# Optimization experiments

Hardware: AMD Instinct MI355X
Metric: run time of the kernel (lower is better)

Reference implementation:

```python
import jax, jax.numpy as jnp
import numpy as np

B, S, H, D, E = 1, 2048, 16, 64, 1024
STRIDE, LCMP = 16, 32          # compression stride / block
LSEL, TOPN = 64, 16            # selection block size / top-k blocks
WIN = 512                      # sliding window
NEG = jnp.float32(-1e9)


def setup_inputs() -> dict:
    key = jax.random.key(0)
    ks = jax.random.split(key, 5)
    q = jax.random.normal(ks[0], (B, S, H, D), jnp.float32)
    k = jax.random.normal(ks[1], (B, S, H, D), jnp.float32)
    v = jax.random.normal(ks[2], (B, S, H, D), jnp.float32)
    x = jax.random.normal(ks[3], (B, S, E), jnp.float32)
    Wg = jax.random.normal(ks[4], (E, 3), jnp.float32) * 0.02
    bg = jnp.zeros((3,), jnp.float32)
    cu_seqlens = jnp.array([0, S], jnp.int32)
    max_seqlen = S
    return {"q": q, "k": k, "v": v, "x": x, "Wg": Wg, "bg": bg,
            "cu_seqlens": cu_seqlens, "max_seqlen": max_seqlen}


def _nsa_forward(q, k, v, x, Wg, bg):
    scale = 1.0 / np.sqrt(D)
    t = jnp.arange(S)
    num_cmp = (S - LCMP) // STRIDE + 1   # 127
    num_sel = S // LSEL                  # 32

    # ---- branch 1: compressed-KV attention (mean-pooled blocks) ----
    starts = jnp.arange(num_cmp) * STRIDE
    widx = starts[:, None] + jnp.arange(LCMP)          # (num_cmp, LCMP)
    Kc = k[:, widx].mean(axis=2)                        # (B, num_cmp, H, D)
    Vc = v[:, widx].mean(axis=2)
    logits_c = jnp.einsum('bshd,bchd->bhsc', q, Kc) * scale
    # query t may attend only to fully-past compressed blocks
    mask_c = (starts + LCMP)[None, :] <= (t[:, None] + 1)   # (S, num_cmp)
    p_c = jax.nn.softmax(jnp.where(mask_c[None, None], logits_c, NEG), axis=-1)
    valid_c = mask_c.any(axis=-1).astype(q.dtype)           # (S,) zero-out empty rows
    p_c = p_c * valid_c[None, None, :, None]
    o_cmp = jnp.einsum('bhsc,bchd->bshd', p_c, Vc)

    # ---- branch 2: top-k selected-block attention ----
    # map compressed-block scores -> selection-block importance (overlap sum)
    sel_s = jnp.arange(num_sel) * LSEL
    overlap = ((starts[:, None] < sel_s[None, :] + LSEL) &
               (starts[:, None] + LCMP > sel_s[None, :])).astype(q.dtype)  # (num_cmp, num_sel)
    p_sel = jnp.einsum('bhsc,cn->bhsn', p_c, overlap)        # (B,H,S,num_sel)
    _, top_idx = jax.lax.top_k(p_sel, TOPN)                  # (B,H,S,TOPN)
    sel_blk = jax.nn.one_hot(top_idx, num_sel).sum(axis=-2) > 0   # (B,H,S,num_sel)
    own_blk = jax.nn.one_hot(t // LSEL, num_sel) > 0              # always include own block
    sel_blk = sel_blk | own_blk[None, None]
    sel_tok = jnp.repeat(sel_blk, LSEL, axis=-1)             # (B,H,S,S) token-level mask

    causal = t[:, None] >= t[None, :]                        # (S,S)
    logits = jnp.einsum('bshd,bthd->bhst', q, k) * scale     # (B,H,S,S), shared by 2 branches
    a_sel = jax.nn.softmax(jnp.where(sel_tok & causal[None, None], logits, NEG), axis=-1)
    o_sel = jnp.einsum('bhst,bthd->bshd', a_sel, v)

    # ---- branch 3: sliding-window attention ----
    win_mask = causal & (t[:, None] - t[None, :] < WIN)
    a_win = jax.nn.softmax(jnp.where(win_mask[None, None], logits, NEG), axis=-1)
    o_win = jnp.einsum('bhst,bthd->bshd', a_win, v)

    # ---- learned gating over the 3 branches ----
    g = jax.nn.sigmoid(x @ Wg + bg)                          # (B,S,3)
    out = (g[..., 0][..., None, None] * o_cmp +
           g[..., 1][..., None, None] * o_sel +
           g[..., 2][..., None, None] * o_win)
    return out                                               # (B,S,H,D)


def reference(q, k, v, x, Wg, bg, cu_seqlens, max_seqlen):
    return _nsa_forward(q, k, v, x, Wg, bg)
```

## Files before the change

### kernel.cpp

```cpp
#include <hip/hip_runtime.h>
#include <hip/hip_bf16.h>
#include <math.h>

#define H_NUM 16
#define D_DIM 64
#define S_LEN 2048
#define E_DIM 1024
#define NC    127
#define TOPN  16
#define SCALE 0.125f
#define FIXM  16.0f
#define LOG2E 1.4426950408889634f
#define C_SC  (SCALE * LOG2E)
#define C_BI  (-FIXM * LOG2E)

typedef short s16x8 __attribute__((ext_vector_type(8)));
typedef short s16x4 __attribute__((ext_vector_type(4)));
typedef float f32x4 __attribute__((ext_vector_type(4)));
typedef unsigned short ushort_t;

__device__ __forceinline__ float fast_exp2(float x) {
    return __builtin_amdgcn_exp2f(x);
}
__device__ __forceinline__ unsigned short f2b(float f) {
    __hip_bfloat16 h = __float2bfloat16(f);
    return *reinterpret_cast<unsigned short*>(&h);
}
__device__ __forceinline__ float b2f(unsigned short u) {
    __hip_bfloat16 h = *reinterpret_cast<__hip_bfloat16*>(&u);
    return __bfloat162float(h);
}
__device__ __forceinline__ s16x8 pack8(float4 a, float4 b) {
    s16x8 r;
    r[0] = (short)f2b(a.x); r[1] = (short)f2b(a.y);
    r[2] = (short)f2b(a.z); r[3] = (short)f2b(a.w);
    r[4] = (short)f2b(b.x); r[5] = (short)f2b(b.y);
    r[6] = (short)f2b(b.z); r[7] = (short)f2b(b.w);
    return r;
}
__device__ __forceinline__ f32x4 mfma16(s16x8 a, s16x8 b, f32x4 c) {
    return __builtin_amdgcn_mfma_f32_16x16x32_bf16(a, b, c, 0, 0, 0);
}
__device__ __forceinline__ void wave_lds_fence() {
    asm volatile("s_waitcnt lgkmcnt(0)" ::: "memory");
    __builtin_amdgcn_sched_barrier(0);
}
__device__ __forceinline__ int swP(int r, int c) { return r * 128 + (c ^ ((r & 7) << 2)); }
__device__ __forceinline__ int swU(int r, int c) { return r * 64  + (c ^ ((r & 7) << 3)); }

__device__ __forceinline__ float wave_sum(float v) {
#pragma unroll
    for (int off = 32; off; off >>= 1) v += __shfl_xor(v, off, 64);
    return v;
}

__global__ __launch_bounds__(256) void nsa_prep(
    const float* __restrict__ k, const float* __restrict__ v,
    const float* __restrict__ x, const float* __restrict__ Wg, const float* __restrict__ bg,
    ushort_t* __restrict__ Kb, ushort_t* __restrict__ VtB,
    ushort_t* __restrict__ KcHi, ushort_t* __restrict__ KcLo, ushort_t* __restrict__ VcT,
    float* __restrict__ g)
{
    const int b   = blockIdx.x;
    const int tid = threadIdx.x;

    if (b < 512) {
        int idx0 = (b * 256 + tid) * 16;
#pragma unroll
        for (int j = 0; j < 16; j += 4) {
            int id = idx0 + j;
            int d = id & 63, s = (id >> 6) & 2047, h = id >> 17;
            float4 f = *(const float4*)(k + ((size_t)s * H_NUM + h) * D_DIM + d);
            s16x4 u;
            u[0] = (short)f2b(f.x); u[1] = (short)f2b(f.y);
            u[2] = (short)f2b(f.z); u[3] = (short)f2b(f.w);
            *(s16x4*)(Kb + id) = u;
        }
    } else if (b < 768) {
        __shared__ ushort_t T[64][136];
        int bb = b - 512;
        int h = bb >> 4, s0 = (bb & 15) << 7;
#pragma unroll
        for (int rep = 0; rep < 8; ++rep) {
            int idx = rep * 256 + tid;
            int i = idx >> 4, d4 = (idx & 15) << 2;
            float4 f = *(const float4*)(v + ((size_t)(s0 + i) * H_NUM + h) * D_DIM + d4);
            T[d4 + 0][i] = f2b(f.x); T[d4 + 1][i] = f2b(f.y);
            T[d4 + 2][i] = f2b(f.z); T[d4 + 3][i] = f2b(f.w);
        }
        __syncthreads();
        int d = tid >> 2, i0 = (tid & 3) << 5;
        ushort_t* dst = VtB + ((size_t)h * 64 + d) * 2048 + s0 + i0;
#pragma unroll
        for (int jj = 0; jj < 32; jj += 8)
            *(s16x8*)(dst + jj) = *(const s16x8*)&T[d][i0 + jj];
    } else if (b < 1280) {
        int unit = (b - 768) * 4 + (tid >> 6);
        int h = unit >> 7, c = unit & 127;
        int lane = tid & 63;
        float mk = 0.f, mv = 0.f;
        if (c < NC) {
            int s0 = c * 16;
#pragma unroll 4
            for (int i = 0; i < 32; ++i) {
                mk += k[((size_t)(s0 + i) * H_NUM + h) * D_DIM + lane];
                mv += v[((size_t)(s0 + i) * H_NUM + h) * D_DIM + lane];
            }
            mk *= (1.f / 32.f); mv *= (1.f / 32.f);
        }
        unsigned short khi = f2b(mk);
        KcHi[((size_t)h * 128 + c) * 64 + lane] = khi;
        KcLo[((size_t)h * 128 + c) * 64 + lane] = f2b(mk - b2f(khi));
        VcT[((size_t)h * 64 + lane) * 128 + c] = f2b(mv);
    } else {
        int s = (b - 1280) * 4 + (tid >> 6);
        int lane = tid & 63;
        float a0 = 0.f, a1 = 0.f, a2 = 0.f;
        for (int i = lane; i < E_DIM; i += 64) {
            float xv = x[(size_t)s * E_DIM + i];
            a0 = fmaf(xv, Wg[i * 3 + 0], a0);
            a1 = fmaf(xv, Wg[i * 3 + 1], a1);
            a2 = fmaf(xv, Wg[i * 3 + 2], a2);
        }
        a0 = wave_sum(a0); a1 = wave_sum(a1); a2 = wave_sum(a2);
        if (lane == 0) {
            g[s * 3 + 0] = 1.f / (1.f + expf(-(a0 + bg[0])));
            g[s * 3 + 1] = 1.f / (1.f + expf(-(a1 + bg[1])));
            g[s * 3 + 2] = 1.f / (1.f + expf(-(a2 + bg[2])));
        }
    }
}

__global__ __launch_bounds__(512, 4) void nsa_main(
    const float* __restrict__ q,
    const ushort_t* __restrict__ Kb, const ushort_t* __restrict__ VtB,
    const ushort_t* __restrict__ KcHi, const ushort_t* __restrict__ KcLo,
    const ushort_t* __restrict__ VcT,
    const float* __restrict__ gat, float* __restrict__ out)
{
    __shared__ __align__(16) float    P1[4 * 2048];
    __shared__ __align__(16) float    psl[4 * 512];
    __shared__ __align__(16) ushort_t BP[4 * 2048];
    __shared__ float    mrg[4 * 32];
    __shared__ unsigned selm_l[64];

    const int bid  = blockIdx.x;
    const int h    = bid & 15;
    const int grp  = bid >> 4;
    const int tile = (grp < 16) ? (31 - grp) : (grp - 16);
    const int t0   = tile << 6;
    const int tid  = threadIdx.x;
    const int w    = tid >> 6;
    const int pair = w & 3;
    const bool isA = w < 4;
    const int lane = tid & 63;
    const int lr   = lane & 15;
    const int g    = lane >> 4;
    const int rb   = t0 + 16 * pair;

    float*    P1w  = P1 + pair * 2048;
    float*    pslw = psl + pair * 512;
    ushort_t* APb  = (ushort_t*)pslw;
    ushort_t* BPw  = BP + pair * 2048;
    float*    mrgw = mrg + pair * 32;

    int trow[4];
#pragma unroll
    for (int r = 0; r < 4; ++r) trow[r] = rb + 4 * g + r;

    s16x8 qa[2], ql[2];
    {
        const float* qrow = q + ((size_t)(rb + lr) * H_NUM + h) * D_DIM;
#pragma unroll
        for (int kk = 0; kk < 2; ++kk) {
            float4 a = *(const float4*)(qrow + kk * 32 + g * 8);
            float4 b = *(const float4*)(qrow + kk * 32 + g * 8 + 4);
            s16x8 hi = pack8(a, b);
            float4 ar, br;
            ar.x = a.x - b2f((unsigned short)hi[0]); ar.y = a.y - b2f((unsigned short)hi[1]);
            ar.z = a.z - b2f((unsigned short)hi[2]); ar.w = a.w - b2f((unsigned short)hi[3]);
            br.x = b.x - b2f((unsigned short)hi[4]); br.y = b.y - b2f((unsigned short)hi[5]);
            br.z = b.z - b2f((unsigned short)hi[6]); br.w = b.w - b2f((unsigned short)hi[7]);
            qa[kk] = hi;
            ql[kk] = pack8(ar, br);
        }
    }

    int nv[4];
#pragma unroll
    for (int r = 0; r < 4; ++r) nv[r] = (trow[r] >= 31) ? (((trow[r] - 31) >> 4) + 1) : 0;

    float l1[4] = {0.f, 0.f, 0.f, 0.f};
    f32x4 oc[4];
#pragma unroll
    for (int dt = 0; dt < 4; ++dt) { f32x4 z = {0.f, 0.f, 0.f, 0.f}; oc[dt] = z; }

    const int winlo = (tile >= 8) ? (tile - 8) : 0;
    float l3[4] = {0.f, 0.f, 0.f, 0.f};
    f32x4 o3[4];
#pragma unroll
    for (int dt = 0; dt < 4; ++dt) { f32x4 z = {0.f, 0.f, 0.f, 0.f}; o3[dt] = z; }

    if (isA) {
        f32x4 sc8[8];
#pragma unroll
        for (int ct = 0; ct < 8; ++ct) {
            f32x4 acc = {0.f, 0.f, 0.f, 0.f};
#pragma unroll
            for (int kk = 0; kk < 2; ++kk) {
                const size_t off = ((size_t)h * 128 + 16 * ct + lr) * 64 + kk * 32 + g * 8;
                s16x8 khi = *(const s16x8*)(KcHi + off);
                s16x8 klo = *(const s16x8*)(KcLo + off);
                acc = mfma16(qa[kk], khi, acc);
                acc = mfma16(ql[kk], khi, acc);
                acc = mfma16(qa[kk], klo, acc);
            }
            sc8[ct] = acc;
        }

#pragma unroll
        for (int ct = 0; ct < 8; ++ct)
#pragma unroll
            for (int r = 0; r < 4; ++r) {
                int c = 16 * ct + lr;
                float p = (c < nv[r]) ? fast_exp2(fmaf(sc8[ct][r], C_SC, C_BI)) : 0.f;
                l1[r] += p;
                P1w[swP(4 * g + r, 16 * ct + lr)] = p;
            }
        wave_lds_fence();

#pragma unroll
        for (int rep = 0; rep < 8; ++rep) {
            int item = rep * 64 + lane;
            int n = item >> 4, row = item & 15;
            int lo = 4 * n - 1; if (lo < 0) lo = 0;
            int hi = 4 * n + 3; if (hi > NC - 1) hi = NC - 1;
            float s = 0.f;
            for (int c = lo; c <= hi; ++c) s += P1w[swP(row, c)];
            pslw[n * 16 + row] = s;
        }
        wave_lds_fence();

        unsigned mymask = 0u;
        {
            float pv[32];
#pragma unroll
            for (int n = 0; n < 32; ++n) pv[n] = (lane < 16) ? pslw[n * 16 + lane] : 0.f;
            for (int it = 0; it < TOPN; ++it) {
                float best = -1.f; int bi = 0;
#pragma unroll
                for (int n = 0; n < 32; ++n) {
                    float val = ((mymask >> n) & 1u) ? -2.f : pv[n];
                    if (val > best) { best = val; bi = n; }
                }
                mymask |= 1u << bi;
            }
        }
        if (lane < 16) selm_l[pair * 16 + lane] = mymask | (1u << tile);

#pragma unroll
        for (int kk = 0; kk < 4; ++kk) {
            float4 a0 = *(const float4*)&P1w[swP(lr, kk * 32 + g * 8)];
            float4 a1 = *(const float4*)&P1w[swP(lr, kk * 32 + g * 8 + 4)];
            s16x8 pa = pack8(a0, a1);
#pragma unroll
            for (int dt = 0; dt < 4; ++dt)
                oc[dt] = mfma16(pa, *(const s16x8*)(VcT + ((size_t)h * 64 + 16 * dt + lr) * 128 + kk * 32 + g * 8), oc[dt]);
        }
#pragma unroll
        for (int off = 8; off >= 1; off >>= 1)
#pragma unroll
            for (int r = 0; r < 4; ++r) l1[r] += __shfl_xor(l1[r], off, 64);
    } else {
        for (int n = winlo; n <= tile; ++n) {
            const int base = n << 6;
            f32x4 s4[4];
#pragma unroll
            for (int ct = 0; ct < 4; ++ct) {
                f32x4 acc = {0.f, 0.f, 0.f, 0.f};
#pragma unroll
                for (int kk = 0; kk < 2; ++kk)
                    acc = mfma16(qa[kk],
                        *(const s16x8*)(Kb + ((size_t)h * 2048 + base + 16 * ct + lr) * 64 + kk * 32 + g * 8), acc);
                s4[ct] = acc;
            }
#pragma unroll
            for (int ct = 0; ct < 4; ++ct)
#pragma unroll
                for (int r = 0; r < 4; ++r) {
                    int j = base + 16 * ct + lr;
                    bool ok = (j >= trow[r] - 511) && (j <= trow[r]);
                    float p = ok ? fast_exp2(fmaf(s4[ct][r], C_SC, C_BI)) : 0.f;
                    l3[r] += p;
                    BPw[swU(4 * g + r, 16 * ct + lr)] = f2b(p);
                }
            wave_lds_fence();
#pragma unroll
            for (int kk = 0; kk < 2; ++kk) {
                s16x8 pa = *(const s16x8*)&BPw[swU(lr, kk * 32 + g * 8)];
#pragma unroll
                for (int dt = 0; dt < 4; ++dt)
                    o3[dt] = mfma16(pa,
                        *(const s16x8*)(VtB + ((size_t)h * 64 + 16 * dt + lr) * 2048 + base + kk * 32 + g * 8), o3[dt]);
            }
        }
#pragma unroll
        for (int off = 8; off >= 1; off >>= 1)
#pragma unroll
            for (int r = 0; r < 4; ++r) l3[r] += __shfl_xor(l3[r], off, 64);
    }
    __syncthreads();

    unsigned um = selm_l[pair * 16 + lr];
#pragma unroll
    for (int off = 8; off >= 1; off >>= 1) um |= __shfl_xor(um, off, 64);
    unsigned selreg[4];
#pragma unroll
    for (int r = 0; r < 4; ++r) selreg[r] = selm_l[pair * 16 + 4 * g + r];

    float l2[4] = {0.f, 0.f, 0.f, 0.f};
    f32x4 o2[4];
#pragma unroll
    for (int dt = 0; dt < 4; ++dt) { f32x4 z = {0.f, 0.f, 0.f, 0.f}; o2[dt] = z; }

    ushort_t* myP = isA ? APb : (BPw + 1024);
    int cnt = 0;
    for (int n = 0; n <= tile; ++n) {
        if (!((um >> n) & 1u)) continue;
        bool mine = ((cnt & 1) == (isA ? 0 : 1));
        ++cnt;
        if (!mine) continue;
        const int base = n << 6;

        f32x4 s4[4];
#pragma unroll
        for (int ct = 0; ct < 4; ++ct) {
            f32x4 acc = {0.f, 0.f, 0.f, 0.f};
#pragma unroll
            for (int kk = 0; kk < 2; ++kk)
                acc = mfma16(qa[kk],
                    *(const s16x8*)(Kb + ((size_t)h * 2048 + base + 16 * ct + lr) * 64 + kk * 32 + g * 8), acc);
            s4[ct] = acc;
        }
#pragma unroll
        for (int ct = 0; ct < 4; ++ct)
#pragma unroll
            for (int r = 0; r < 4; ++r) {
                int j = base + 16 * ct + lr;
                bool ok = ((selreg[r] >> n) & 1u) && (j <= trow[r]);
                float p = ok ? fast_exp2(fmaf(s4[ct][r], C_SC, C_BI)) : 0.f;
                l2[r] += p;
                myP[swU(4 * g + r, 16 * ct + lr)] = f2b(p);
            }
        wave_lds_fence();
#pragma unroll
        for (int kk = 0; kk < 2; ++kk) {
            s16x8 pa = *(const s16x8*)&myP[swU(lr, kk * 32 + g * 8)];
#pragma unroll
            for (int dt = 0; dt < 4; ++dt)
                o2[dt] = mfma16(pa,
                    *(const s16x8*)(VtB + ((size_t)h * 64 + 16 * dt + lr) * 2048 + base + kk * 32 + g * 8), o2[dt]);
        }
    }
#pragma unroll
    for (int off = 8; off >= 1; off >>= 1)
#pragma unroll
        for (int r = 0; r < 4; ++r) l2[r] += __shfl_xor(l2[r], off, 64);

    if (!isA) {
#pragma unroll
        for (int dt = 0; dt < 4; ++dt)
#pragma unroll
            for (int r = 0; r < 4; ++r) {
                P1w[(4 * g + r) * 64 + 16 * dt + lr] = o2[dt][r];
                P1w[1024 + (4 * g + r) * 64 + 16 * dt + lr] = o3[dt][r];
            }
        if (lr == 0)
#pragma unroll
            for (int r = 0; r < 4; ++r) {
                mrgw[(4 * g + r) * 2 + 0] = l2[r];
                mrgw[(4 * g + r) * 2 + 1] = l3[r];
            }
    }
    __syncthreads();

    if (isA) {
#pragma unroll
        for (int r = 0; r < 4; ++r) {
            const int row = 4 * g + r;
            float l2f = l2[r] + mrgw[row * 2 + 0];
            float l3B = mrgw[row * 2 + 1];
            const float* gp = gat + (size_t)trow[r] * 3;
            float g0 = gp[0], g1 = gp[1], g2 = gp[2];
            float invc = nv[r] ? (1.f / l1[r]) : 0.f;
            float i2 = 1.f / l2f, i3 = 1.f / l3B;
#pragma unroll
            for (int dt = 0; dt < 4; ++dt) {
                float o2f = o2[dt][r] + P1w[row * 64 + 16 * dt + lr];
                float o3f = P1w[1024 + row * 64 + 16 * dt + lr];
                float val = g0 * (oc[dt][r] * invc) + g1 * (o2f * i2) + g2 * (o3f * i3);
                out[((size_t)trow[r] * H_NUM + h) * D_DIM + 16 * dt + lr] = val;
            }
        }
    }
}

extern "C" void kernel_launch(void* const* d_in, const int* in_sizes, int n_in,
                              void* d_out, int out_size, void* d_ws, size_t ws_size,
                              hipStream_t stream) {
    const float* q  = (const float*)d_in[0];
    const float* k  = (const float*)d_in[1];
    const float* v  = (const float*)d_in[2];
    const float* x  = (const float*)d_in[3];
    const float* Wg = (const float*)d_in[4];
    const float* bg = (const float*)d_in[5];
    float* out = (float*)d_out;

    ushort_t* Kb   = (ushort_t*)d_ws;
    ushort_t* VtB  = Kb  + (size_t)16 * 2048 * 64;
    ushort_t* KcHi = VtB + (size_t)16 * 64 * 2048;
    ushort_t* KcLo = KcHi + (size_t)16 * 128 * 64;
    ushort_t* VcT  = KcLo + (size_t)16 * 128 * 64;
    float*    g    = (float*)(VcT + (size_t)16 * 64 * 128);

    nsa_prep<<<1792, 256, 0, stream>>>(k, v, x, Wg, bg, Kb, VtB, KcHi, KcLo, VcT, g);
    nsa_main<<<512, 512, 0, stream>>>(q, Kb, VtB, KcHi, KcLo, VcT, g, out);
}
```

Baseline: 126.5 us.

## Split main kernel work across four wave roles with 1024-thread blocks

```diff
diff --git a/kernel.cpp b/kernel.cpp
--- a/kernel.cpp
+++ b/kernel.cpp
@@ -19,9 +19,7 @@
 typedef float f32x4 __attribute__((ext_vector_type(4)));
 typedef unsigned short ushort_t;
 
-__device__ __forceinline__ float fast_exp2(float x) {
-    return __builtin_amdgcn_exp2f(x);
-}
+__device__ __forceinline__ float fast_exp2(float x) { return __builtin_amdgcn_exp2f(x); }
 __device__ __forceinline__ unsigned short f2b(float f) {
     __hip_bfloat16 h = __float2bfloat16(f);
     return *reinterpret_cast<unsigned short*>(&h);
@@ -52,6 +50,27 @@
 #pragma unroll
     for (int off = 32; off; off >>= 1) v += __shfl_xor(v, off, 64);
     return v;
+}
+
+__device__ __forceinline__ f32x4 qk_ct(const ushort_t* __restrict__ KbH, const s16x8 qa[2],
+                                       int base, int ct, int lr, int g) {
+    f32x4 acc = {0.f, 0.f, 0.f, 0.f};
+#pragma unroll
+    for (int kk = 0; kk < 2; ++kk)
+        acc = mfma16(qa[kk],
+            *(const s16x8*)(KbH + (size_t)(base + 16 * ct + lr) * 64 + kk * 32 + g * 8), acc);
+    return acc;
+}
+__device__ __forceinline__ void pv_block(const ushort_t* __restrict__ VtBH, const ushort_t* Pb,
+                                         int base, int lr, int g, f32x4 o[4]) {
+#pragma unroll
+    for (int kk = 0; kk < 2; ++kk) {
+        s16x8 pa = *(const s16x8*)&Pb[swU(lr, kk * 32 + g * 8)];
+#pragma unroll
+        for (int dt = 0; dt < 4; ++dt)
+            o[dt] = mfma16(pa,
+                *(const s16x8*)(VtBH + (size_t)(16 * dt + lr) * 2048 + base + kk * 32 + g * 8), o[dt]);
+    }
 }
 
 __global__ __launch_bounds__(256) void nsa_prep(
@@ -131,7 +150,7 @@
     }
 }
 
-__global__ __launch_bounds__(512, 4) void nsa_main(
+__global__ __launch_bounds__(1024, 8) void nsa_main(
     const float* __restrict__ q,
     const ushort_t* __restrict__ Kb, const ushort_t* __restrict__ VtB,
     const ushort_t* __restrict__ KcHi, const ushort_t* __restrict__ KcLo,
@@ -139,9 +158,9 @@
     const float* __restrict__ gat, float* __restrict__ out)
 {
     __shared__ __align__(16) float    P1[4 * 2048];
+    __shared__ __align__(16) ushort_t BP[4 * 3072];
     __shared__ __align__(16) float    psl[4 * 512];
-    __shared__ __align__(16) ushort_t BP[4 * 2048];
-    __shared__ float    mrg[4 * 32];
+    __shared__ float    mrg[4 * 128];
     __shared__ unsigned selm_l[64];
 
     const int bid  = blockIdx.x;
@@ -152,17 +171,21 @@
     const int tid  = threadIdx.x;
     const int w    = tid >> 6;
     const int pair = w & 3;
-    const bool isA = w < 4;
+    const int role = w >> 2;
     const int lane = tid & 63;
     const int lr   = lane & 15;
     const int g    = lane >> 4;
     const int rb   = t0 + 16 * pair;
 
     float*    P1w  = P1 + pair * 2048;
+    ushort_t* P1u  = (ushort_t*)P1w;
+    ushort_t* BPw  = BP + pair * 3072;
     float*    pslw = psl + pair * 512;
-    ushort_t* APb  = (ushort_t*)pslw;
-    ushort_t* BPw  = BP + pair * 2048;
-    float*    mrgw = mrg + pair * 32;
+    ushort_t* ocst = (ushort_t*)pslw;
+    float*    mrgw = mrg + pair * 128;
+
+    const ushort_t* KbH  = Kb  + (size_t)h * 2048 * 64;
+    const ushort_t* VtBH = VtB + (size_t)h * 64 * 2048;
 
     int trow[4];
 #pragma unroll
@@ -176,13 +199,15 @@
             float4 a = *(const float4*)(qrow + kk * 32 + g * 8);
             float4 b = *(const float4*)(qrow + kk * 32 + g * 8 + 4);
             s16x8 hi = pack8(a, b);
-            float4 ar, br;
-            ar.x = a.x - b2f((unsigned short)hi[0]); ar.y = a.y - b2f((unsigned short)hi[1]);
-            ar.z = a.z - b2f((unsigned short)hi[2]); ar.w = a.w - b2f((unsigned short)hi[3]);
-            br.x = b.x - b2f((unsigned short)hi[4]); br.y = b.y - b2f((unsigned short)hi[5]);
-            br.z = b.z - b2f((unsigned short)hi[6]); br.w = b.w - b2f((unsigned short)hi[7]);
             qa[kk] = hi;
-            ql[kk] = pack8(ar, br);
+            if (role == 0) {
+                float4 ar, br;
+                ar.x = a.x - b2f((unsigned short)hi[0]); ar.y = a.y - b2f((unsigned short)hi[1]);
+                ar.z = a.z - b2f((unsigned short)hi[2]); ar.w = a.w - b2f((unsigned short)hi[3]);
+                br.x = b.x - b2f((unsigned short)hi[4]); br.y = b.y - b2f((unsigned short)hi[5]);
+                br.z = b.z - b2f((unsigned short)hi[6]); br.w = b.w - b2f((unsigned short)hi[7]);
+                ql[kk] = pack8(ar, br);
+            }
         }
     }
 
@@ -190,20 +215,10 @@
 #pragma unroll
     for (int r = 0; r < 4; ++r) nv[r] = (trow[r] >= 31) ? (((trow[r] - 31) >> 4) + 1) : 0;
 
+    const int winlo = (tile >= 8) ? (tile - 8) : 0;
     float l1[4] = {0.f, 0.f, 0.f, 0.f};
-    f32x4 oc[4];
-#pragma unroll
-    for (int dt = 0; dt < 4; ++dt) { f32x4 z = {0.f, 0.f, 0.f, 0.f}; oc[dt] = z; }
-
-    const int winlo = (tile >= 8) ? (tile - 8) : 0;
-    float l3[4] = {0.f, 0.f, 0.f, 0.f};
-    f32x4 o3[4];
-#pragma unroll
-    for (int dt = 0; dt < 4; ++dt) { f32x4 z = {0.f, 0.f, 0.f, 0.f}; o3[dt] = z; }
-
-    if (isA) {
-        f32x4 sc8[8];
-#pragma unroll
+
+    if (role == 0) {
         for (int ct = 0; ct < 8; ++ct) {
             f32x4 acc = {0.f, 0.f, 0.f, 0.f};
 #pragma unroll
@@ -215,18 +230,14 @@
                 acc = mfma16(ql[kk], khi, acc);
                 acc = mfma16(qa[kk], klo, acc);
             }
-            sc8[ct] = acc;
-        }
-
-#pragma unroll
-        for (int ct = 0; ct < 8; ++ct)
 #pragma unroll
             for (int r = 0; r < 4; ++r) {
                 int c = 16 * ct + lr;
-                float p = (c < nv[r]) ? fast_exp2(fmaf(sc8[ct][r], C_SC, C_BI)) : 0.f;
+                float p = (c < nv[r]) ? fast_exp2(fmaf(acc[r], C_SC, C_BI)) : 0.f;
                 l1[r] += p;
-                P1w[swP(4 * g + r, 16 * ct + lr)] = p;
-            }
+                P1w[swP(4 * g + r, c)] = p;
+            }
+        }
         wave_lds_fence();
 
 #pragma unroll
@@ -258,6 +269,9 @@
         }
         if (lane < 16) selm_l[pair * 16 + lane] = mymask | (1u << tile);
 
+        f32x4 oc[4];
+#pragma unroll
+        for (int dt = 0; dt < 4; ++dt) { f32x4 z = {0.f, 0.f, 0.f, 0.f}; oc[dt] = z; }
 #pragma unroll
         for (int kk = 0; kk < 4; ++kk) {
             float4 a0 = *(const float4*)&P1w[swP(lr, kk * 32 + g * 8)];
@@ -271,43 +285,48 @@
         for (int off = 8; off >= 1; off >>= 1)
 #pragma unroll
             for (int r = 0; r < 4; ++r) l1[r] += __shfl_xor(l1[r], off, 64);
+        wave_lds_fence();
+#pragma unroll
+        for (int dt = 0; dt < 4; ++dt)
+#pragma unroll
+            for (int r = 0; r < 4; ++r)
+                ocst[(4 * g + r) * 64 + 16 * dt + lr] = f2b(oc[dt][r]);
     } else {
-        for (int n = winlo; n <= tile; ++n) {
+        float l3[4] = {0.f, 0.f, 0.f, 0.f};
+        f32x4 o3[4];
+#pragma unroll
+        for (int dt = 0; dt < 4; ++dt) { f32x4 z = {0.f, 0.f, 0.f, 0.f}; o3[dt] = z; }
+        ushort_t* WP = BPw + (role - 1) * 1024;
+        for (int n = winlo + role - 1; n <= tile; n += 3) {
             const int base = n << 6;
-            f32x4 s4[4];
 #pragma unroll
             for (int ct = 0; ct < 4; ++ct) {
-                f32x4 acc = {0.f, 0.f, 0.f, 0.f};
-#pragma unroll
-                for (int kk = 0; kk < 2; ++kk)
-                    acc = mfma16(qa[kk],
-                        *(const s16x8*)(Kb + ((size_t)h * 2048 + base + 16 * ct + lr) * 64 + kk * 32 + g * 8), acc);
-                s4[ct] = acc;
-            }
-#pragma unroll
-            for (int ct = 0; ct < 4; ++ct)
+                f32x4 acc = qk_ct(KbH, qa, base, ct, lr, g);
 #pragma unroll
                 for (int r = 0; r < 4; ++r) {
                     int j = base + 16 * ct + lr;
                     bool ok = (j >= trow[r] - 511) && (j <= trow[r]);
-                    float p = ok ? fast_exp2(fmaf(s4[ct][r], C_SC, C_BI)) : 0.f;
+                    float p = ok ? fast_exp2(fmaf(acc[r], C_SC, C_BI)) : 0.f;
                     l3[r] += p;
-                    BPw[swU(4 * g + r, 16 * ct + lr)] = f2b(p);
+                    WP[swU(4 * g + r, 16 * ct + lr)] = f2b(p);
                 }
+            }
             wave_lds_fence();
-#pragma unroll
-            for (int kk = 0; kk < 2; ++kk) {
-                s16x8 pa = *(const s16x8*)&BPw[swU(lr, kk * 32 + g * 8)];
-#pragma unroll
-                for (int dt = 0; dt < 4; ++dt)
-                    o3[dt] = mfma16(pa,
-                        *(const s16x8*)(VtB + ((size_t)h * 64 + 16 * dt + lr) * 2048 + base + kk * 32 + g * 8), o3[dt]);
-            }
+            pv_block(VtBH, WP, base, lr, g, o3);
         }
 #pragma unroll
         for (int off = 8; off >= 1; off >>= 1)
 #pragma unroll
             for (int r = 0; r < 4; ++r) l3[r] += __shfl_xor(l3[r], off, 64);
+        wave_lds_fence();
+#pragma unroll
+        for (int dt = 0; dt < 4; ++dt)
+#pragma unroll
+            for (int r = 0; r < 4; ++r)
+                WP[(4 * g + r) * 64 + 16 * dt + lr] = f2b(o3[dt][r]);
+        if (lr == 0)
+#pragma unroll
+            for (int r = 0; r < 4; ++r) mrgw[(4 * g + r) * 6 + 3 + (role - 1)] = l3[r];
     }
     __syncthreads();
 
@@ -323,82 +342,64 @@
 #pragma unroll
     for (int dt = 0; dt < 4; ++dt) { f32x4 z = {0.f, 0.f, 0.f, 0.f}; o2[dt] = z; }
 
-    ushort_t* myP = isA ? APb : (BPw + 1024);
+    ushort_t* myP = P1u + role * 1024;
     int cnt = 0;
     for (int n = 0; n <= tile; ++n) {
         if (!((um >> n) & 1u)) continue;
-        bool mine = ((cnt & 1) == (isA ? 0 : 1));
+        bool mine = (cnt & 3) == role;
         ++cnt;
         if (!mine) continue;
         const int base = n << 6;
-
-        f32x4 s4[4];
 #pragma unroll
         for (int ct = 0; ct < 4; ++ct) {
-            f32x4 acc = {0.f, 0.f, 0.f, 0.f};
-#pragma unroll
-            for (int kk = 0; kk < 2; ++kk)
-                acc = mfma16(qa[kk],
-                    *(const s16x8*)(Kb + ((size_t)h * 2048 + base + 16 * ct + lr) * 64 + kk * 32 + g * 8), acc);
-            s4[ct] = acc;
-        }
-#pragma unroll
-        for (int ct = 0; ct < 4; ++ct)
+            f32x4 acc = qk_ct(KbH, qa, base, ct, lr, g);
 #pragma unroll
             for (int r = 0; r < 4; ++r) {
                 int j = base + 16 * ct + lr;
                 bool ok = ((selreg[r] >> n) & 1u) && (j <= trow[r]);
-                float p = ok ? fast_exp2(fmaf(s4[ct][r], C_SC, C_BI)) : 0.f;
+                float p = ok ? fast_exp2(fmaf(acc[r], C_SC, C_BI)) : 0.f;
                 l2[r] += p;
                 myP[swU(4 * g + r, 16 * ct + lr)] = f2b(p);
             }
-        wave_lds_fence();
-#pragma unroll
-        for (int kk = 0; kk < 2; ++kk) {
-            s16x8 pa = *(const s16x8*)&myP[swU(lr, kk * 32 + g * 8)];
-#pragma unroll
-            for (int dt = 0; dt < 4; ++dt)
-                o2[dt] = mfma16(pa,
-                    *(const s16x8*)(VtB + ((size_t)h * 64 + 16 * dt + lr) * 2048 + base + kk * 32 + g * 8), o2[dt]);
-        }
+        }
+        wave_lds_fence();
+        pv_block(VtBH, myP, base, lr, g, o2);
     }
 #pragma unroll
     for (int off = 8; off >= 1; off >>= 1)
 #pragma unroll
         for (int r = 0; r < 4; ++r) l2[r] += __shfl_xor(l2[r], off, 64);
 
-    if (!isA) {
+    if (role != 0) {
+        wave_lds_fence();
 #pragma unroll
         for (int dt = 0; dt < 4; ++dt)
 #pragma unroll
-            for (int r = 0; r < 4; ++r) {
-                P1w[(4 * g + r) * 64 + 16 * dt + lr] = o2[dt][r];
-                P1w[1024 + (4 * g + r) * 64 + 16 * dt + lr] = o3[dt][r];
-            }
+            for (int r = 0; r < 4; ++r)
+                myP[(4 * g + r) * 64 + 16 * dt + lr] = f2b(o2[dt][r]);
         if (lr == 0)
 #pragma unroll
-            for (int r = 0; r < 4; ++r) {
-                mrgw[(4 * g + r) * 2 + 0] = l2[r];
-                mrgw[(4 * g + r) * 2 + 1] = l3[r];
-            }
+            for (int r = 0; r < 4; ++r) mrgw[(4 * g + r) * 6 + (role - 1)] = l2[r];
     }
     __syncthreads();
 
-    if (isA) {
+    if (role == 0) {
 #pragma unroll
         for (int r = 0; r < 4; ++r) {
             const int row = 4 * g + r;
-            float l2f = l2[r] + mrgw[row * 2 + 0];
-            float l3B = mrgw[row * 2 + 1];
+            float l2f = l2[r] + mrgw[row * 6 + 0] + mrgw[row * 6 + 1] + mrgw[row * 6 + 2];
+            float l3f = mrgw[row * 6 + 3] + mrgw[row * 6 + 4] + mrgw[row * 6 + 5];
             const float* gp = gat + (size_t)trow[r] * 3;
             float g0 = gp[0], g1 = gp[1], g2 = gp[2];
             float invc = nv[r] ? (1.f / l1[r]) : 0.f;
-            float i2 = 1.f / l2f, i3 = 1.f / l3B;
+            float i2 = 1.f / l2f, i3 = 1.f / l3f;
 #pragma unroll
             for (int dt = 0; dt < 4; ++dt) {
-                float o2f = o2[dt][r] + P1w[row * 64 + 16 * dt + lr];
-                float o3f = P1w[1024 + row * 64 + 16 * dt + lr];
-                float val = g0 * (oc[dt][r] * invc) + g1 * (o2f * i2) + g2 * (o3f * i3);
+                const int idx = row * 64 + 16 * dt + lr;
+                float o2f = o2[dt][r] + b2f(P1u[1024 + idx]) + b2f(P1u[2048 + idx]) + b2f(P1u[3072 + idx]);
+                float o3f = b2f(BPw[idx]) + b2f(BPw[1024 + idx]) + b2f(BPw[2048 + idx]);
+                float ocf = b2f(ocst[idx]);
+                float val = g0 * (ocf * invc) + g1 * (o2f * i2) + g2 * (o3f * i3);
                 out[((size_t)trow[r] * H_NUM + h) * D_DIM + 16 * dt + lr] = val;
             }
         }
@@ -424,5 +425,5 @@
     float*    g    = (float*)(VcT + (size_t)16 * 64 * 128);
 
     nsa_prep<<<1792, 256, 0, stream>>>(k, v, x, Wg, bg, Kb, VtB, KcHi, KcLo, VcT, g);
-    nsa_main<<<512, 512, 0, stream>>>(q, Kb, VtB, KcHi, KcLo, VcT, g, out);
-}
+    nsa_main<<<512, 1024, 0, stream>>>(q, Kb, VtB, KcHi, KcLo, VcT, g, out);
+}
```

After: 208.4 us. +64.8%, slower.
